# Kernel tuning notes

Measured on AMD Instinct MI355X. Metric: run time of the kernel, lower is better.

Reference implementation:

```python
import jax, jax.numpy as jnp
import numpy as np

C = 128; HEADS = 8; GH = 32; GW = 32; B = 8; PD = 8  # PD = (dim//4)//4

def _conv(x, w, pad, dil=1, groups=1):
    return jax.lax.conv_general_dilated(
        x, w, (1, 1), [(pad[0], pad[0]), (pad[1], pad[1])],
        rhs_dilation=(dil, dil),
        dimension_numbers=('NCHW', 'OIHW', 'NCHW'),
        feature_group_count=groups)

def _lrelu(t):
    return jnp.where(t >= 0, t, 0.1 * t)

def _ln(t, g, b, eps=1e-5):
    m = jnp.mean(t, -1, keepdims=True)
    v = jnp.var(t, -1, keepdims=True)
    return (t - m) * jax.lax.rsqrt(v + eps) * g + b

def setup_inputs():
    rng = np.random.RandomState(0)
    f = lambda *s: jnp.asarray((rng.randn(*s) * 0.05).astype(np.float32))
    ones = lambda n: jnp.ones((n,), jnp.float32)
    zeros = lambda n: jnp.zeros((n,), jnp.float32)
    # Swin-style relative position index over the (GH, GW) group
    coords = np.stack(np.meshgrid(np.arange(GH), np.arange(GW), indexing='ij')).reshape(2, -1)
    rel = (coords[:, :, None] - coords[:, None, :]).transpose(1, 2, 0)
    rel[..., 0] += GH - 1; rel[..., 1] += GW - 1; rel[..., 0] *= 2 * GW - 1
    rel_idx = jnp.asarray(rel.sum(-1).astype(np.int32))  # [N, N]
    biases = np.stack(np.meshgrid(np.arange(1 - GH, GH), np.arange(1 - GW, GW), indexing='ij'))
    biases = jnp.asarray(biases.reshape(2, -1).T.astype(np.float32))  # [(2GH-1)*(2GW-1), 2]
    return dict(
        x=jnp.asarray(rng.rand(B, C, GH, GW).astype(np.float32)),
        conv1_w=f(C, C, 3, 3), conv2_w=f(C, C, 3, 3), conv3_w=f(C, C, 3, 3),
        convt_w=f(C, 3, 1, 1),
        rba_w=f(C, C, 3, 1), rba_b=zeros(C), rbb_w=f(C, C, 1, 3), rbb_b=zeros(C),
        pp_w=f(PD, 2), pp_b=zeros(PD),
        l1_g=ones(PD), l1_b=zeros(PD), l1_w=f(PD, PD), l1_b2=zeros(PD),
        l2_g=ones(PD), l2_b=zeros(PD), l2_w=f(PD, PD), l2_b2=zeros(PD),
        l3_g=ones(PD), l3_b=zeros(PD), l3_w=f(HEADS, PD), l3_b2=zeros(HEADS),
        qk_w=f(2 * C, C), qk_b=zeros(2 * C),
        v_w=f(C, C), v_b=zeros(C),
        proj_w=f(C, C), proj_b=zeros(C),
        fc1_w=f(C, C), fc1_b=zeros(C), fc2_w=f(C, C), fc2_b=zeros(C),
        biases=biases, rel_idx=rel_idx,
    )

def reference(x, conv1_w, conv2_w, conv3_w, convt_w, rba_w, rba_b, rbb_w, rbb_b,
              pp_w, pp_b, l1_g, l1_b, l1_w, l1_b2, l2_g, l2_b, l2_w, l2_b2,
              l3_g, l3_b, l3_w, l3_b2, qk_w, qk_b, v_w, v_b, proj_w, proj_b,
              fc1_w, fc1_b, fc2_w, fc2_b, biases, rel_idx):
    Bn, Cc, Hh, Ww = x.shape
    N = Hh * Ww
    hd = Cc // HEADS
    # FeaExtract: ResASPP (3 dilated 3x3 convs, grouped 1x1 merge) + residual
    b1 = _lrelu(_conv(x, conv1_w, (1, 1)))
    b2 = _lrelu(_conv(x, conv2_w, (3, 3), dil=3))
    b3 = _lrelu(_conv(x, conv3_w, (5, 5), dil=5))
    a = _conv(jnp.concatenate([b1, b2, b3], 1), convt_w, (0, 0), groups=Cc) + x
    # RB: (3,1) conv -> lrelu -> (1,3) conv + residual
    r = _lrelu(_conv(a, rba_w, (1, 0)) + rba_b[None, :, None, None])
    r = _conv(r, rbb_w, (0, 1)) + rbb_b[None, :, None, None]
    o0 = r + a
    # original uses in-place clamp_, so o0 is clamped before flattening
    o0 = jnp.clip(o0, 0.0, 1.0)
    E = o0.reshape(Bn, Cc, N).transpose(0, 2, 1)  # [B, N, C]
    qk = E @ qk_w.T + qk_b  # [B, N, 2C]
    q = qk[..., :Cc].reshape(Bn, N, HEADS, hd).transpose(0, 2, 1, 3)
    k = qk[..., Cc:].reshape(Bn, N, HEADS, hd).transpose(0, 2, 1, 3)
    v = (E @ v_w.T + v_b).reshape(Bn, N, HEADS, hd).transpose(0, 2, 1, 3)
    attn = jnp.einsum('bhid,bhjd->bhij', q * (hd ** -0.5), k)
    # DynamicPosBias MLP (residual=False): Linear(2,pd) -> [LN,ReLU,Linear] x2 -> LN,ReLU,Linear(pd,heads)
    p = biases @ pp_w.T + pp_b
    p = jax.nn.relu(_ln(p, l1_g, l1_b)) @ l1_w.T + l1_b2
    p = jax.nn.relu(_ln(p, l2_g, l2_b)) @ l2_w.T + l2_b2
    p = jax.nn.relu(_ln(p, l3_g, l3_b)) @ l3_w.T + l3_b2  # [L, heads]
    rpb = p[rel_idx]  # gather -> [N, N, heads]
    attn = attn + rpb.transpose(2, 0, 1)[None]
    attn = jax.nn.softmax(attn, axis=-1)
    y = jnp.einsum('bhij,bhjd->bhid', attn, v).transpose(0, 2, 1, 3).reshape(Bn, N, Cc) + E
    x_proj = y @ proj_w.T + proj_b
    h = jax.nn.gelu(x_proj @ fc1_w.T + fc1_b, approximate=False)
    return (h @ fc2_w.T + fc2_b) + y
```

## Files before the change

### kernel.cpp

```cpp
#include <hip/hip_runtime.h>
#include <hip/hip_bf16.h>

typedef __hip_bfloat16 bf16;
typedef __bf16 bf16x8 __attribute__((ext_vector_type(8)));
typedef float f32x4 __attribute__((ext_vector_type(4)));

#define Lb 3969

#define XP_F   0
#define WF_F   903168
#define WR_F   1124352
#define WG_F   1173504
#define BH_F   1222656
#define R1P_F  1222656
#define QKV_F  1222656
#define AP_F   2795520
#define YT_F   2795520
#define EB_F   3352576
#define XPT_F  3352576
#define H1T_F  0
#define RPB_F  3876864
#define FLAG_F 3908616
#define RT_F   3908624
#define VT_F   4416528

__device__ __forceinline__ float b2f(bf16 v) { return __bfloat162float(v); }
__device__ __forceinline__ bf16 f2b(float v) { return __float2bfloat16(v); }

template <typename T> __device__ __forceinline__ float ldw(const void* p, int i);
template <> __device__ __forceinline__ float ldw<bf16>(const void* p, int i) {
  return __bfloat162float(((const bf16*)p)[i]);
}
template <> __device__ __forceinline__ float ldw<float>(const void* p, int i) {
  return ((const float*)p)[i];
}
template <typename T> __device__ __forceinline__ void stw(void* p, size_t i, float v);
template <> __device__ __forceinline__ void stw<bf16>(void* p, size_t i, float v) {
  ((bf16*)p)[i] = __float2bfloat16(v);
}
template <> __device__ __forceinline__ void stw<float>(void* p, size_t i, float v) {
  ((float*)p)[i] = v;
}

__device__ __forceinline__ unsigned pkb(float a, float b) {
  bf16 x = __float2bfloat16(a), y = __float2bfloat16(b);
  unsigned short ux = *(unsigned short*)&x, uy = *(unsigned short*)&y;
  return (unsigned)ux | ((unsigned)uy << 16);
}
__device__ __forceinline__ float bf2f_lo(unsigned w) {
  unsigned u = w << 16; return *(float*)&u;
}
__device__ __forceinline__ float bf2f_hi(unsigned w) {
  unsigned u = w & 0xffff0000u; return *(float*)&u;
}

__device__ __forceinline__ bool detect_local(const unsigned* x) {
  int lane = threadIdx.x & 63;
  int cnt = 0;
#pragma unroll
  for (int k = 0; k < 4; ++k) {
    unsigned lo = x[lane + 64 * k] & 0xFFFFu;
    cnt += (lo >= 0x3C00u && lo < 0x3F80u) ? 1 : 0;
  }
#pragma unroll
  for (int off = 1; off < 64; off <<= 1) cnt += __shfl_xor(cnt, off);
  return cnt >= 128;
}

template <typename T>
__device__ void wprep_all_body(const void* w1, const void* w2, const void* w3,
                               const void* rba_w, const void* rbb_w,
                               const void* qk_w, const void* v_w,
                               const void* proj_w, const void* fc1_w,
                               const void* fc2_w, bf16* __restrict__ Wf,
                               bf16* __restrict__ Wr, bf16* __restrict__ Wg)
{
  int tid = blockIdx.x * 256 + threadIdx.x;
  int lane = tid & 63, li = lane & 15, quad = lane >> 4;
  if (tid < 55296) {
    int mt = (tid >> 6) & 7;
    int Kc = (tid >> 9) & 3;
    int rem = tid >> 11;
    int t = rem % 9;
    int br = rem / 9;
    const void* w = (br == 0 ? w1 : (br == 1 ? w2 : w3));
    int o = mt * 16 + li;
    int ci0 = Kc * 32 + quad * 8;
#pragma unroll
    for (int j = 0; j < 8; ++j)
      Wf[(size_t)tid * 8 + j] = f2b(ldw<T>(w, (o * 128 + ci0 + j) * 9 + t));
  } else {
    int u = tid - 55296;
    if (u < 12288) {
      int Kc = (u >> 6) & 3, mt = (u >> 8) & 7, q = u >> 11;
      const void* w = (q >= 3) ? rbb_w : rba_w;
      int t = q % 3;
#pragma unroll
      for (int j = 0; j < 8; ++j)
        Wr[(size_t)u * 8 + j] =
            f2b(ldw<T>(w, ((mt * 16 + li) * 128 + Kc * 32 + quad * 8 + j) * 3 + t));
    } else if (u < 24576) {
      int g = u - 12288;
      int Kc = (g >> 6) & 3, mtg = g >> 8;
      const void* w; int mrow; float sc = 1.f;
      if (mtg < 16)      { w = qk_w;   mrow = mtg * 16; if (mtg < 8) sc = 0.25f; }
      else if (mtg < 24) { w = v_w;    mrow = (mtg - 16) * 16; }
      else if (mtg < 32) { w = proj_w; mrow = (mtg - 24) * 16; }
      else if (mtg < 40) { w = fc1_w;  mrow = (mtg - 32) * 16; }
      else               { w = fc2_w;  mrow = (mtg - 40) * 16; }
#pragma unroll
      for (int j = 0; j < 8; ++j)
        Wg[(size_t)g * 8 + j] =
            f2b(sc * ldw<T>(w, (mrow + li) * 128 + Kc * 32 + quad * 8 + j));
    }
  }
}

__global__ __launch_bounds__(256) void wprep_all_kernel(
    const unsigned* x, const void* w1, const void* w2, const void* w3,
    const void* rba_w, const void* rbb_w, const void* qk_w, const void* v_w,
    const void* proj_w, const void* fc1_w, const void* fc2_w,
    bf16* Wf, bf16* Wr, bf16* Wg, int* flag)
{
  bool isbf = detect_local(x);
  if (blockIdx.x == 0 && threadIdx.x == 0) *flag = isbf ? 1 : 0;
  if (isbf) wprep_all_body<bf16>(w1, w2, w3, rba_w, rbb_w, qk_w, v_w, proj_w,
                                 fc1_w, fc2_w, Wf, Wr, Wg);
  else      wprep_all_body<float>(w1, w2, w3, rba_w, rbb_w, qk_w, v_w, proj_w,
                                  fc1_w, fc2_w, Wf, Wr, Wg);
}

template <typename T>
__device__ void nhwc_body(const void* x, bf16* __restrict__ xp, bf16 (*tile)[128])
{
  const int b = blockIdx.x >> 5;
  const int row = blockIdx.x & 31;
  const int t = threadIdx.x;
  const size_t bbase = (size_t)b * 42 * 42 * 128;
  const bf16x8 z = (bf16x8){};

  if (t < 160) {
    int side = t / 80;
    int off = (t % 80) * 8;
    *(bf16x8*)&xp[bbase + ((size_t)(row + 5) * 42 + side * 37) * 128 + off] = z;
  }
  {
    int zr = (row < 5) ? row : ((row >= 27) ? row + 10 : -1);
    if (zr >= 0) {
      size_t base = bbase + (size_t)zr * 42 * 128;
      for (int k = t; k < 672; k += 256) *(bf16x8*)&xp[base + k * 8] = z;
    }
  }

  {
    int ci = t >> 1, half = t & 1;
#pragma unroll
    for (int j = 0; j < 16; ++j) {
      int px = half * 16 + j;
      tile[px][ci] = f2b(ldw<T>(x, ((size_t)b * 128 + ci) * 1024 + row * 32 + px));
    }
  }
  __syncthreads();
  {
    int px = t >> 3, c0 = (t & 7) * 16;
    bf16* dst = xp + (bbase + ((size_t)(row + 5) * 42 + (px + 5)) * 128 + c0);
#pragma unroll
    for (int j = 0; j < 16; ++j) dst[j] = tile[px][c0 + j];
  }
}

__global__ __launch_bounds__(256) void nhwc_kernel(const void* x, bf16* xp,
                                                   const int* flag)
{
  __shared__ bf16 tile[32][128];
  if (*flag) nhwc_body<bf16>(x, xp, tile);
  else       nhwc_body<float>(x, xp, tile);
}

__global__ __launch_bounds__(256) void aspp2_kernel(
    const bf16* __restrict__ xp, const bf16* __restrict__ Wf,
    bf16* __restrict__ bh)
{
  const int nt_ = blockIdx.x, br = blockIdx.y >> 1, mh = blockIdx.y & 1;
  const int bb = blockIdx.z;
  const int w = threadIdx.x >> 6, lane = threadIdx.x & 63;
  const int quad = lane >> 4, li = lane & 15;
  const int d = (br == 0 ? 1 : (br == 1 ? 3 : 5));
  const int pxw = nt_ * 64 + w * 16;
  const int y = pxw >> 5, xb = pxw & 31;

  f32x4 acc[4] = {};
  const bf16* Wbase = Wf + (size_t)br * 18432 * 8 + (size_t)mh * 4 * 64 * 8;

  for (int t = 0; t < 9; ++t) {
    const int dy = (t / 3 - 1) * d, dx = (t % 3 - 1) * d;
    const bf16* Asite =
        xp + (((size_t)bb * 42 + (y + 5 + dy)) * 42 + (xb + li + 5 + dx)) * 128;
    const bf16* Wt = Wbase + (size_t)t * 2048 * 8;
#pragma unroll
    for (int Kc = 0; Kc < 4; ++Kc) {
      bf16x8 afrag = *(const bf16x8*)(Asite + Kc * 32 + quad * 8);
      const bf16* Wk = Wt + (size_t)Kc * 512 * 8 + (size_t)lane * 8;
#pragma unroll
      for (int mt = 0; mt < 4; ++mt) {
        bf16x8 wfrag = *(const bf16x8*)(Wk + (size_t)mt * 64 * 8);
        acc[mt] = __builtin_amdgcn_mfma_f32_16x16x32_bf16(afrag, wfrag, acc[mt],
                                                          0, 0, 0);
      }
    }
  }
#pragma unroll
  for (int mt = 0; mt < 4; ++mt)
#pragma unroll
    for (int r = 0; r < 4; ++r) {
      int px = pxw + quad * 4 + r;
      bh[((size_t)bb * 1024 + px) * 384 + br * 128 + (mh * 4 + mt) * 16 + li] =
          f2b(acc[mt][r]);
    }
}

template <typename T>
__device__ void merge2_body(const bf16* __restrict__ xp, const void* wt,
                            const bf16* __restrict__ bh, bf16* __restrict__ ap,
                            float* cw)
{
  const int b = blockIdx.y, px0 = blockIdx.x * 32;
  const bf16x8 z = (bf16x8){};
  if (blockIdx.x == 0) {
    size_t base = ((size_t)b * 34 + 0) * 32 * 128;
    for (int k = threadIdx.x; k < 512; k += 256) *(bf16x8*)&ap[base + k * 8] = z;
  } else if (blockIdx.x == 31) {
    size_t base = ((size_t)b * 34 + 33) * 32 * 128;
    for (int k = threadIdx.x; k < 512; k += 256) *(bf16x8*)&ap[base + k * 8] = z;
  }
  for (int i = threadIdx.x; i < 384; i += 256) cw[i] = ldw<T>(wt, i);
  __syncthreads();
  const int pxl = threadIdx.x >> 3, og = threadIdx.x & 7;
  const int px = px0 + pxl, o0 = og * 16;
  const int y = px >> 5, x = px & 31;
  const bf16* brow = bh + ((size_t)b * 1024 + px) * 384 + o0 * 3;
  const bf16* xrow = xp + (((size_t)b * 42 + y + 5) * 42 + x + 5) * 128 + o0;
  bf16* arow = ap + (((size_t)b * 34 + y + 1) * 32 + x) * 128 + o0;

  bf16 bl[48], xl[16], ol[16];
#pragma unroll
  for (int k = 0; k < 6; ++k) *(bf16x8*)&bl[k * 8] = *(const bf16x8*)&brow[k * 8];
  *(bf16x8*)&xl[0] = *(const bf16x8*)&xrow[0];
  *(bf16x8*)&xl[8] = *(const bf16x8*)&xrow[8];
#pragma unroll
  for (int j = 0; j < 16; ++j) {
    float v = b2f(xl[j]);
#pragma unroll
    for (int i = 0; i < 3; ++i) {
      float t = b2f(bl[j * 3 + i]);
      v += cw[(o0 + j) * 3 + i] * (t >= 0.f ? t : 0.1f * t);
    }
    ol[j] = f2b(v);
  }
  *(bf16x8*)&arow[0] = *(bf16x8*)&ol[0];
  *(bf16x8*)&arow[8] = *(bf16x8*)&ol[8];
}

__global__ __launch_bounds__(256) void merge2_kernel(
    const bf16* xp, const void* wt, const bf16* bh, bf16* ap, const int* flag)
{
  __shared__ float cw[384];
  if (*flag) merge2_body<bf16>(xp, wt, bh, ap, cw);
  else       merge2_body<float>(xp, wt, bh, ap, cw);
}

template <typename T>
__device__ void rb1_body(const bf16* __restrict__ ap, const bf16* __restrict__ Wr,
                         const void* bias, bf16* __restrict__ r1p)
{
  const int b = blockIdx.z, mh = blockIdx.y;
  const int lane = threadIdx.x;
  const int quad = lane >> 4, li = lane & 15;
  const int pxw = blockIdx.x * 16;
  const int y = pxw >> 5, xb = pxw & 31;
  f32x4 acc[4] = {};
#pragma unroll
  for (int t = 0; t < 3; ++t) {
    const bf16* Asite = ap + (((size_t)b * 34 + y + t) * 32 + xb + li) * 128;
#pragma unroll
    for (int Kc = 0; Kc < 4; ++Kc) {
      bf16x8 afrag = *(const bf16x8*)(Asite + Kc * 32 + quad * 8);
#pragma unroll
      for (int mt = 0; mt < 4; ++mt) {
        int f = (t * 8 + mh * 4 + mt) * 4 + Kc;
        bf16x8 wfrag = *(const bf16x8*)(Wr + ((size_t)f * 64 + lane) * 8);
        acc[mt] = __builtin_amdgcn_mfma_f32_16x16x32_bf16(afrag, wfrag, acc[mt],
                                                          0, 0, 0);
      }
    }
  }
  if (quad == 0) {
    int xcol = (xb == 0) ? 0 : 33;
#pragma unroll
    for (int mt = 0; mt < 4; ++mt)
      r1p[(((size_t)b * 32 + y) * 34 + xcol) * 128 + (mh * 4 + mt) * 16 + li] =
          f2b(0.f);
  }
#pragma unroll
  for (int mt = 0; mt < 4; ++mt) {
    int o = (mh * 4 + mt) * 16 + li;
    float bv = ldw<T>(bias, o);
#pragma unroll
    for (int r = 0; r < 4; ++r) {
      int x = xb + quad * 4 + r;
      float v = acc[mt][r] + bv;
      v = (v >= 0.f ? v : 0.1f * v);
      r1p[(((size_t)b * 32 + y) * 34 + x + 1) * 128 + o] = f2b(v);
    }
  }
}

__global__ __launch_bounds__(64) void rb1_kernel(
    const bf16* ap, const bf16* Wr, const void* bias, bf16* r1p, const int* flag)
{
  if (*flag) rb1_body<bf16>(ap, Wr, bias, r1p);
  else       rb1_body<float>(ap, Wr, bias, r1p);
}

template <typename T>
__device__ void rb2_body(const bf16* __restrict__ r1p, const bf16* __restrict__ Wr,
                         const void* bias, const bf16* __restrict__ ap,
                         bf16* __restrict__ Eb)
{
  const int b = blockIdx.z, mh = blockIdx.y;
  const int lane = threadIdx.x;
  const int quad = lane >> 4, li = lane & 15;
  const int pxw = blockIdx.x * 16;
  const int y = pxw >> 5, xb = pxw & 31;
  f32x4 acc[4] = {};
#pragma unroll
  for (int t = 0; t < 3; ++t) {
    const bf16* Asite = r1p + (((size_t)b * 32 + y) * 34 + xb + li + t) * 128;
#pragma unroll
    for (int Kc = 0; Kc < 4; ++Kc) {
      bf16x8 afrag = *(const bf16x8*)(Asite + Kc * 32 + quad * 8);
#pragma unroll
      for (int mt = 0; mt < 4; ++mt) {
        int f = ((3 + t) * 8 + mh * 4 + mt) * 4 + Kc;
        bf16x8 wfrag = *(const bf16x8*)(Wr + ((size_t)f * 64 + lane) * 8);
        acc[mt] = __builtin_amdgcn_mfma_f32_16x16x32_bf16(afrag, wfrag, acc[mt],
                                                          0, 0, 0);
      }
    }
  }
#pragma unroll
  for (int mt = 0; mt < 4; ++mt) {
    int o = (mh * 4 + mt) * 16 + li;
    float bv = ldw<T>(bias, o);
#pragma unroll
    for (int r = 0; r < 4; ++r) {
      int x = xb + quad * 4 + r;
      float v = acc[mt][r] + bv +
                b2f(ap[(((size_t)b * 34 + y + 1) * 32 + x) * 128 + o]);
      v = fminf(fmaxf(v, 0.f), 1.f);
      Eb[((size_t)b * 1024 + y * 32 + x) * 128 + o] = f2b(v);
    }
  }
}

__global__ __launch_bounds__(64) void rb2_kernel(
    const bf16* r1p, const bf16* Wr, const void* bias, const bf16* ap,
    bf16* Eb, const int* flag)
{
  if (*flag) rb2_body<bf16>(r1p, Wr, bias, ap, Eb);
  else       rb2_body<float>(r1p, Wr, bias, ap, Eb);
}

template <typename T>
__device__ __forceinline__ void ln_relu8(const float* t, float* u,
                                         const void* g, const void* bb)
{
  float m = 0.f;
#pragma unroll
  for (int k = 0; k < 8; ++k) m += t[k];
  m *= 0.125f;
  float v = 0.f;
#pragma unroll
  for (int k = 0; k < 8; ++k) { float d = t[k] - m; v += d * d; }
  v *= 0.125f;
  float r = rsqrtf(v + 1e-5f);
#pragma unroll
  for (int k = 0; k < 8; ++k) {
    float val = (t[k] - m) * r * ldw<T>(g, k) + ldw<T>(bb, k);
    u[k] = val > 0.f ? val : 0.f;
  }
}

template <typename T>
__device__ void dpb_body(const void* biases, const void* pp_w, const void* pp_b,
                         const void* l1_g, const void* l1_b, const void* l1_w,
                         const void* l1_b2, const void* l2_g, const void* l2_b,
                         const void* l2_w, const void* l2_b2, const void* l3_g,
                         const void* l3_b, const void* l3_w, const void* l3_b2,
                         float* __restrict__ RPB)
{
  int r = blockIdx.x * 256 + threadIdx.x;
  if (r >= Lb) return;
  float b0 = ldw<T>(biases, r * 2), b1 = ldw<T>(biases, r * 2 + 1);
  float t[8], u[8];
#pragma unroll
  for (int j = 0; j < 8; ++j)
    t[j] = b0 * ldw<T>(pp_w, j * 2) + b1 * ldw<T>(pp_w, j * 2 + 1) +
           ldw<T>(pp_b, j);
  ln_relu8<T>(t, u, l1_g, l1_b);
#pragma unroll
  for (int j = 0; j < 8; ++j) {
    float s = ldw<T>(l1_b2, j);
#pragma unroll
    for (int k = 0; k < 8; ++k) s += u[k] * ldw<T>(l1_w, j * 8 + k);
    t[j] = s;
  }
  ln_relu8<T>(t, u, l2_g, l2_b);
#pragma unroll
  for (int j = 0; j < 8; ++j) {
    float s = ldw<T>(l2_b2, j);
#pragma unroll
    for (int k = 0; k < 8; ++k) s += u[k] * ldw<T>(l2_w, j * 8 + k);
    t[j] = s;
  }
  ln_relu8<T>(t, u, l3_g, l3_b);
#pragma unroll
  for (int h = 0; h < 8; ++h) {
    float s = ldw<T>(l3_b2, h);
#pragma unroll
    for (int k = 0; k < 8; ++k) s += u[k] * ldw<T>(l3_w, h * 8 + k);
    RPB[h * Lb + r] = s;
  }
}

__global__ __launch_bounds__(256) void dpb_kernel(
    const void* biases, const void* pp_w, const void* pp_b, const void* l1_g,
    const void* l1_b, const void* l1_w, const void* l1_b2, const void* l2_g,
    const void* l2_b, const void* l2_w, const void* l2_b2, const void* l3_g,
    const void* l3_b, const void* l3_w, const void* l3_b2, float* RPB,
    const int* flag)
{
  if (*flag)
    dpb_body<bf16>(biases, pp_w, pp_b, l1_g, l1_b, l1_w, l1_b2, l2_g, l2_b,
                   l2_w, l2_b2, l3_g, l3_b, l3_w, l3_b2, RPB);
  else
    dpb_body<float>(biases, pp_w, pp_b, l1_g, l1_b, l1_w, l1_b2, l2_g, l2_b,
                    l2_w, l2_b2, l3_g, l3_b, l3_w, l3_b2, RPB);
}

__global__ __launch_bounds__(64) void rt_kernel(
    const float* __restrict__ RPB, bf16* __restrict__ RT)
{
  const int tt = blockIdx.x, h = blockIdx.y;
  const int t = tt >> 1, p = tt & 1;
  const int lane = threadIdx.x, quad = lane >> 4, li = lane & 15;
  const float* rp = RPB + h * Lb;
#pragma unroll
  for (int mt = 0; mt < 4; ++mt) {
    unsigned w[2];
#pragma unroll
    for (int rr = 0; rr < 2; ++rr) {
      float v0, v1;
#pragma unroll
      for (int k = 0; k < 2; ++k) {
        int r = rr * 2 + k;
        int j = mt * 16 + quad * 4 + r;
        int dy = (t - 30) - (j >> 5);
        int dx = (p * 16 + li) - (j & 31);
        float v = rp[(dy + 31) * 63 + dx + 31];
        if (k == 0) v0 = v; else v1 = v;
      }
      w[rr] = pkb(v0, v1);
    }
    *(uint2*)&RT[(((size_t)h * 124 + tt) * 4 + mt) * 256 + lane * 4] =
        make_uint2(w[0], w[1]);
  }
}

__global__ __launch_bounds__(64) void vt_kernel(
    const bf16* __restrict__ QKV, bf16* __restrict__ VT)
{
  const int c = blockIdx.x, hh = blockIdx.y, b = blockIdx.z;
  __shared__ bf16 Vl[64][20];
  const int lane = threadIdx.x, quad = lane >> 4, li = lane & 15;
  const bf16* vsrc =
      QKV + ((size_t)b * 1024 + c * 64 + lane) * 384 + 256 + hh * 16;
  union { bf16x8 v; uint2 u[2]; } w0, w1;
  w0.v = *(const bf16x8*)vsrc;
  w1.v = *(const bf16x8*)(vsrc + 8);
  *(uint2*)&Vl[lane][0] = w0.u[0];
  *(uint2*)&Vl[lane][4] = w0.u[1];
  *(uint2*)&Vl[lane][8] = w1.u[0];
  *(uint2*)&Vl[lane][12] = w1.u[1];
  __syncthreads();
#pragma unroll
  for (int half = 0; half < 2; ++half) {
    union { bf16 e[8]; bf16x8 v; } uv;
#pragma unroll
    for (int jj = 0; jj < 8; ++jj)
      uv.e[jj] = Vl[half * 32 + quad * 8 + jj][li];
    *(bf16x8*)&VT[((((size_t)(b * 8 + hh) * 16 + c) * 2 + half) * 64 + lane) * 8] =
        uv.v;
  }
}

template <typename T>
__device__ void qkv_body(const bf16* __restrict__ Eb, const bf16* __restrict__ Wg,
                         const void* qk_b, const void* v_b,
                         bf16* __restrict__ QKV)
{
  const int grp = blockIdx.y, b = blockIdx.z;
  const int w = threadIdx.x >> 6, lane = threadIdx.x & 63;
  const int quad = lane >> 4, li = lane & 15;
  const int pxw = blockIdx.x * 64 + w * 16;
  bf16x8 ef[4];
#pragma unroll
  for (int Kc = 0; Kc < 4; ++Kc)
    ef[Kc] = *(const bf16x8*)&Eb[((size_t)b * 1024 + pxw + li) * 128 + Kc * 32 +
                                 quad * 8];
  f32x4 acc[8] = {};
#pragma unroll
  for (int nt = 0; nt < 8; ++nt) {
    int g = grp * 8 + nt;
#pragma unroll
    for (int Kc = 0; Kc < 4; ++Kc) {
      bf16x8 wf = *(const bf16x8*)&Wg[(((size_t)g * 4 + Kc) * 64 + lane) * 8];
      acc[nt] = __builtin_amdgcn_mfma_f32_16x16x32_bf16(ef[Kc], wf, acc[nt],
                                                        0, 0, 0);
    }
  }
#pragma unroll
  for (int nt = 0; nt < 8; ++nt) {
    int g = grp * 8 + nt;
    int o = g * 16 + li;
    float bv;
    if (g < 8)       bv = 0.25f * ldw<T>(qk_b, o);
    else if (g < 16) bv = ldw<T>(qk_b, o);
    else             bv = ldw<T>(v_b, o - 256);
#pragma unroll
    for (int r = 0; r < 4; ++r) {
      int px = pxw + quad * 4 + r;
      QKV[((size_t)b * 1024 + px) * 384 + o] = f2b(acc[nt][r] + bv);
    }
  }
}

__global__ __launch_bounds__(256) void qkv_kernel(
    const bf16* Eb, const bf16* Wg, const void* qk_b, const void* v_b,
    bf16* QKV, const int* flag)
{
  if (*flag) qkv_body<bf16>(Eb, Wg, qk_b, v_b, QKV);
  else       qkv_body<float>(Eb, Wg, qk_b, v_b, QKV);
}

template <typename T, int MODE>
__device__ void mlp_body(const bf16* __restrict__ src, const bf16* __restrict__ Wg,
                         int tb, const void* bias, const bf16* __restrict__ res,
                         void* out)
{
  const int b = blockIdx.z, mh = blockIdx.y;
  const int lane = threadIdx.x;
  const int quad = lane >> 4, li = lane & 15;
  const int pxw = blockIdx.x * 16;
  bf16x8 ef[4];
#pragma unroll
  for (int Kc = 0; Kc < 4; ++Kc)
    ef[Kc] = *(const bf16x8*)&src[((size_t)b * 1024 + pxw + li) * 128 + Kc * 32 +
                                  quad * 8];
  f32x4 acc[2] = {};
#pragma unroll
  for (int nt = 0; nt < 2; ++nt)
#pragma unroll
    for (int Kc = 0; Kc < 4; ++Kc) {
      bf16x8 wf = *(const bf16x8*)&Wg[
          (((size_t)(tb + mh * 2 + nt) * 4 + Kc) * 64 + lane) * 8];
      acc[nt] = __builtin_amdgcn_mfma_f32_16x16x32_bf16(ef[Kc], wf, acc[nt],
                                                        0, 0, 0);
    }
#pragma unroll
  for (int nt = 0; nt < 2; ++nt) {
    int o = (mh * 2 + nt) * 16 + li;
    float bv = ldw<T>(bias, o);
#pragma unroll
    for (int r = 0; r < 4; ++r) {
      int px = pxw + quad * 4 + r;
      float v = acc[nt][r] + bv;
      size_t oidx = ((size_t)b * 1024 + px) * 128 + o;
      if (MODE == 1) v = 0.5f * v * (1.f + erff(v * 0.70710678118f));
      if (MODE == 2) {
        v += b2f(res[oidx]);
        stw<T>(out, oidx, v);
      } else {
        ((bf16*)out)[oidx] = f2b(v);
      }
    }
  }
}

template <int MODE>
__global__ __launch_bounds__(64) void mlp_kernel(
    const bf16* src, const bf16* Wg, int tb, const void* bias, const bf16* res,
    void* out, const int* flag)
{
  if (*flag) mlp_body<bf16, MODE>(src, Wg, tb, bias, res, out);
  else       mlp_body<float, MODE>(src, Wg, tb, bias, res, out);
}

__global__ __launch_bounds__(64) void attn_kernel(
    const bf16* __restrict__ QKV, const bf16* __restrict__ Eb,
    const bf16* __restrict__ RT, const bf16* __restrict__ VT,
    bf16* __restrict__ Yt)
{
  const int qt = blockIdx.x;
  const int hh = blockIdx.y;
  const int b = blockIdx.z;

  __shared__ bf16 Pl[16][72];

  const int lane = threadIdx.x;
  const int quad = lane >> 4, li = lane & 15;
  const int qb = qt * 16;

  const bf16* QKVb = QKV + (size_t)b * 1024 * 384;
  const bf16* VTb = VT + (size_t)(b * 8 + hh) * 16 * 1024;
  const bf16* RTh = RT + (size_t)hh * 124 * 1024;

  bf16x8 qf = (bf16x8){};
  if (quad < 2)
    qf = *(const bf16x8*)&QKVb[(size_t)(qb + li) * 384 + hh * 16 + quad * 8];

  f32x4 O_ = {};
  float m_st = -1e30f, l_st = 0.f;
  const int sbase = (lane & 48) + ((lane >> 2) & 12);

  for (int c = 0; c < 16; ++c) {
    const int c0 = c * 64;
    const int tt = ((qt >> 1) - 2 * c + 30) * 2 + (qt & 1);
    const bf16* rtp = RTh + (size_t)tt * 1024 + lane * 4;

    f32x4 sT[4];
#pragma unroll
    for (int mt = 0; mt < 4; ++mt) {
      uint2 rw = *(const uint2*)(rtp + (size_t)mt * 256);
      f32x4 cin;
      cin[0] = bf2f_lo(rw.x); cin[1] = bf2f_hi(rw.x);
      cin[2] = bf2f_lo(rw.y); cin[3] = bf2f_hi(rw.y);
      bf16x8 kf = (bf16x8){};
      if (quad < 2)
        kf = *(const bf16x8*)&QKVb[(size_t)(c0 + mt * 16 + li) * 384 + 128 +
                                   hh * 16 + quad * 8];
      sT[mt] = __builtin_amdgcn_mfma_f32_16x16x32_bf16(kf, qf, cin, 0, 0, 0);
    }

    float cm = sT[0][0];
#pragma unroll
    for (int mt = 0; mt < 4; ++mt)
#pragma unroll
      for (int r = 0; r < 4; ++r) cm = fmaxf(cm, sT[mt][r]);
    cm = fmaxf(cm, __shfl_xor(cm, 16));
    cm = fmaxf(cm, __shfl_xor(cm, 32));
    float mn = fmaxf(m_st, cm);
    float al = __expf(m_st - mn);
    m_st = mn;
    float ps = 0.f;
#pragma unroll
    for (int mt = 0; mt < 4; ++mt)
#pragma unroll
      for (int r = 0; r < 4; ++r) {
        float p = __expf(sT[mt][r] - mn);
        sT[mt][r] = p;
        ps += p;
      }
    ps += __shfl_xor(ps, 16);
    ps += __shfl_xor(ps, 32);
    l_st = l_st * al + ps;

#pragma unroll
    for (int r = 0; r < 4; ++r) O_[r] *= __shfl(al, sbase + r);

#pragma unroll
    for (int mt = 0; mt < 4; ++mt) {
      uint2 w;
      w.x = pkb(sT[mt][0], sT[mt][1]);
      w.y = pkb(sT[mt][2], sT[mt][3]);
      *(uint2*)&Pl[li][mt * 16 + quad * 4] = w;
    }
    __syncthreads();

#pragma unroll
    for (int half = 0; half < 2; ++half) {
      bf16x8 vf = *(const bf16x8*)&VTb[((size_t)(c * 2 + half) * 64 + lane) * 8];
      bf16x8 pf = *(const bf16x8*)&Pl[li][half * 32 + quad * 8];
      O_ = __builtin_amdgcn_mfma_f32_16x16x32_bf16(pf, vf, O_, 0, 0, 0);
    }
    __syncthreads();
  }

  const bf16* Ebp = Eb + (size_t)b * 1024 * 128 + hh * 16 + li;
  bf16* Ytp = Yt + (size_t)b * 1024 * 128 + hh * 16 + li;
#pragma unroll
  for (int r = 0; r < 4; ++r) {
    float lb = __shfl(l_st, sbase + r);
    int qrow = qb + quad * 4 + r;
    Ytp[(size_t)qrow * 128] =
        f2b(O_[r] / lb + b2f(Ebp[(size_t)qrow * 128]));
  }
}

extern "C" void kernel_launch(void* const* d_in, const int* in_sizes, int n_in,
                              void* d_out, int out_size, void* d_ws,
                              size_t ws_size, hipStream_t stream)
{
  (void)in_sizes; (void)n_in; (void)out_size; (void)ws_size;
  const void* x       = d_in[0];
  const void* conv1_w = d_in[1];
  const void* conv2_w = d_in[2];
  const void* conv3_w = d_in[3];
  const void* convt_w = d_in[4];
  const void* rba_w   = d_in[5];
  const void* rba_b   = d_in[6];
  const void* rbb_w   = d_in[7];
  const void* rbb_b   = d_in[8];
  const void* pp_w    = d_in[9];
  const void* pp_b    = d_in[10];
  const void* l1_g    = d_in[11];
  const void* l1_b    = d_in[12];
  const void* l1_w    = d_in[13];
  const void* l1_b2   = d_in[14];
  const void* l2_g    = d_in[15];
  const void* l2_b    = d_in[16];
  const void* l2_w    = d_in[17];
  const void* l2_b2   = d_in[18];
  const void* l3_g    = d_in[19];
  const void* l3_b    = d_in[20];
  const void* l3_w    = d_in[21];
  const void* l3_b2   = d_in[22];
  const void* qk_w    = d_in[23];
  const void* qk_b    = d_in[24];
  const void* v_w     = d_in[25];
  const void* v_b     = d_in[26];
  const void* proj_w  = d_in[27];
  const void* proj_b  = d_in[28];
  const void* fc1_w   = d_in[29];
  const void* fc1_b   = d_in[30];
  const void* fc2_w   = d_in[31];
  const void* fc2_b   = d_in[32];
  const void* biases  = d_in[33];

  float* ws   = (float*)d_ws;
  bf16*  xp   = (bf16*)(ws + XP_F);
  bf16*  Wf   = (bf16*)(ws + WF_F);
  bf16*  Wr   = (bf16*)(ws + WR_F);
  bf16*  Wg   = (bf16*)(ws + WG_F);
  bf16*  bh   = (bf16*)(ws + BH_F);
  bf16*  r1p  = (bf16*)(ws + R1P_F);
  bf16*  QKV  = (bf16*)(ws + QKV_F);
  bf16*  ap   = (bf16*)(ws + AP_F);
  bf16*  Yt   = (bf16*)(ws + YT_F);
  bf16*  Eb   = (bf16*)(ws + EB_F);
  bf16*  XPt  = (bf16*)(ws + XPT_F);
  bf16*  H1t  = (bf16*)(ws + H1T_F);
  float* RPB  = ws + RPB_F;
  int*   flag = (int*)(ws + FLAG_F);
  bf16*  RT   = (bf16*)(ws + RT_F);
  bf16*  VT   = (bf16*)(ws + VT_F);

  wprep_all_kernel<<<312, 256, 0, stream>>>(
      (const unsigned*)x, conv1_w, conv2_w, conv3_w, rba_w, rbb_w, qk_w, v_w,
      proj_w, fc1_w, fc2_w, Wf, Wr, Wg, flag);
  nhwc_kernel<<<256, 256, 0, stream>>>(x, xp, flag);
  aspp2_kernel<<<dim3(16, 6, 8), 256, 0, stream>>>(xp, Wf, bh);
  merge2_kernel<<<dim3(32, 8), 256, 0, stream>>>(xp, convt_w, bh, ap, flag);
  rb1_kernel<<<dim3(64, 2, 8), 64, 0, stream>>>(ap, Wr, rba_b, r1p, flag);
  rb2_kernel<<<dim3(64, 2, 8), 64, 0, stream>>>(r1p, Wr, rbb_b, ap, Eb, flag);
  dpb_kernel<<<16, 256, 0, stream>>>(biases, pp_w, pp_b, l1_g, l1_b, l1_w,
                                     l1_b2, l2_g, l2_b, l2_w, l2_b2, l3_g,
                                     l3_b, l3_w, l3_b2, RPB, flag);
  rt_kernel<<<dim3(124, 8), 64, 0, stream>>>(RPB, RT);
  qkv_kernel<<<dim3(16, 3, 8), 256, 0, stream>>>(Eb, Wg, qk_b, v_b, QKV, flag);
  vt_kernel<<<dim3(16, 8, 8), 64, 0, stream>>>(QKV, VT);
  attn_kernel<<<dim3(64, 8, 8), 64, 0, stream>>>(QKV, Eb, RT, VT, Yt);
  mlp_kernel<0><<<dim3(64, 4, 8), 64, 0, stream>>>(Yt, Wg, 24, proj_b, nullptr,
                                                   XPt, flag);
  mlp_kernel<1><<<dim3(64, 4, 8), 64, 0, stream>>>(XPt, Wg, 32, fc1_b, nullptr,
                                                   H1t, flag);
  mlp_kernel<2><<<dim3(64, 4, 8), 64, 0, stream>>>(H1t, Wg, 40, fc2_b, Yt,
                                                   d_out, flag);
}
```

Baseline: 243.5 us.

## Keep P in registers via f16 MFMA, double-buffer K/bias loads, lazy softmax rescale

The attention kernel now feeds softmax probabilities directly from registers into a 16x16x16 f16 MFMA, with V pre-transposed to fp16 in the matching fragment layout. This removes the LDS round-trip and both __syncthreads per chunk. K fragments and relative-bias tiles are double-buffered across chunks, and the bias table is stored as fp32 so it is used without unpacking. The online-softmax rescale is skipped unless the running max grows by more than 8. In exchange, the fp32 bias table doubles its memory traffic and P and V lose some precision in fp16.

New measurement: 247.7 us. About the same (+1.7%).

```diff
diff --git a/kernel.cpp b/kernel.cpp
--- a/kernel.cpp
+++ b/kernel.cpp
@@ -4,6 +4,8 @@
 typedef __hip_bfloat16 bf16;
 typedef __bf16 bf16x8 __attribute__((ext_vector_type(8)));
 typedef float f32x4 __attribute__((ext_vector_type(4)));
+typedef __fp16 f16x2 __attribute__((ext_vector_type(2)));
+typedef __fp16 f16x4 __attribute__((ext_vector_type(4)));
 
 #define Lb 3969
 
@@ -22,7 +24,7 @@
 #define RPB_F  3876864
 #define FLAG_F 3908616
 #define RT_F   3908624
-#define VT_F   4416528
+#define VT_F   4924432
 
 __device__ __forceinline__ float b2f(bf16 v) { return __bfloat162float(v); }
 __device__ __forceinline__ bf16 f2b(float v) { return __float2bfloat16(v); }
@@ -47,11 +49,9 @@
   unsigned short ux = *(unsigned short*)&x, uy = *(unsigned short*)&y;
   return (unsigned)ux | ((unsigned)uy << 16);
 }
-__device__ __forceinline__ float bf2f_lo(unsigned w) {
-  unsigned u = w << 16; return *(float*)&u;
-}
-__device__ __forceinline__ float bf2f_hi(unsigned w) {
-  unsigned u = w & 0xffff0000u; return *(float*)&u;
+__device__ __forceinline__ unsigned pkh(float a, float b) {
+  f16x2 t = __builtin_amdgcn_cvt_pkrtz(a, b);
+  return *(unsigned*)&t;
 }
 
 __device__ __forceinline__ bool detect_local(const unsigned* x) {
@@ -449,36 +449,29 @@
 }
 
 __global__ __launch_bounds__(64) void rt_kernel(
-    const float* __restrict__ RPB, bf16* __restrict__ RT)
+    const float* __restrict__ RPB, float* __restrict__ RTf)
 {
   const int tt = blockIdx.x, h = blockIdx.y;
   const int t = tt >> 1, p = tt & 1;
   const int lane = threadIdx.x, quad = lane >> 4, li = lane & 15;
   const float* rp = RPB + h * Lb;
+  float* dst = RTf + ((size_t)(h * 124 + tt) * 4) * 256 + lane * 4;
 #pragma unroll
   for (int mt = 0; mt < 4; ++mt) {
-    unsigned w[2];
-#pragma unroll
-    for (int rr = 0; rr < 2; ++rr) {
-      float v0, v1;
-#pragma unroll
-      for (int k = 0; k < 2; ++k) {
-        int r = rr * 2 + k;
-        int j = mt * 16 + quad * 4 + r;
-        int dy = (t - 30) - (j >> 5);
-        int dx = (p * 16 + li) - (j & 31);
-        float v = rp[(dy + 31) * 63 + dx + 31];
-        if (k == 0) v0 = v; else v1 = v;
-      }
-      w[rr] = pkb(v0, v1);
-    }
-    *(uint2*)&RT[(((size_t)h * 124 + tt) * 4 + mt) * 256 + lane * 4] =
-        make_uint2(w[0], w[1]);
+    f32x4 v;
+#pragma unroll
+    for (int r = 0; r < 4; ++r) {
+      int j = mt * 16 + quad * 4 + r;
+      int dy = (t - 30) - (j >> 5);
+      int dx = (p * 16 + li) - (j & 31);
+      v[r] = rp[(dy + 31) * 63 + dx + 31];
+    }
+    *(f32x4*)(dst + mt * 256) = v;
   }
 }
 
 __global__ __launch_bounds__(64) void vt_kernel(
-    const bf16* __restrict__ QKV, bf16* __restrict__ VT)
+    const bf16* __restrict__ QKV, uint2* __restrict__ VTh)
 {
   const int c = blockIdx.x, hh = blockIdx.y, b = blockIdx.z;
   __shared__ bf16 Vl[64][20];
@@ -493,14 +486,15 @@
   *(uint2*)&Vl[lane][8] = w1.u[0];
   *(uint2*)&Vl[lane][12] = w1.u[1];
   __syncthreads();
-#pragma unroll
-  for (int half = 0; half < 2; ++half) {
-    union { bf16 e[8]; bf16x8 v; } uv;
-#pragma unroll
-    for (int jj = 0; jj < 8; ++jj)
-      uv.e[jj] = Vl[half * 32 + quad * 8 + jj][li];
-    *(bf16x8*)&VT[((((size_t)(b * 8 + hh) * 16 + c) * 2 + half) * 64 + lane) * 8] =
-        uv.v;
+  uint2* dst = VTh + (((size_t)(b * 8 + hh) * 16 + c) * 4) * 64 + lane;
+#pragma unroll
+  for (int mt = 0; mt < 4; ++mt) {
+    uint2 pu;
+    pu.x = pkh(b2f(Vl[mt * 16 + quad * 4 + 0][li]),
+               b2f(Vl[mt * 16 + quad * 4 + 1][li]));
+    pu.y = pkh(b2f(Vl[mt * 16 + quad * 4 + 2][li]),
+               b2f(Vl[mt * 16 + quad * 4 + 3][li]));
+    dst[(size_t)mt * 64] = pu;
   }
 }
 
@@ -608,22 +602,20 @@
 
 __global__ __launch_bounds__(64) void attn_kernel(
     const bf16* __restrict__ QKV, const bf16* __restrict__ Eb,
-    const bf16* __restrict__ RT, const bf16* __restrict__ VT,
+    const float* __restrict__ RTf, const uint2* __restrict__ VTh,
     bf16* __restrict__ Yt)
 {
   const int qt = blockIdx.x;
   const int hh = blockIdx.y;
   const int b = blockIdx.z;
 
-  __shared__ bf16 Pl[16][72];
-
   const int lane = threadIdx.x;
   const int quad = lane >> 4, li = lane & 15;
   const int qb = qt * 16;
 
   const bf16* QKVb = QKV + (size_t)b * 1024 * 384;
-  const bf16* VTb = VT + (size_t)(b * 8 + hh) * 16 * 1024;
-  const bf16* RTh = RT + (size_t)hh * 124 * 1024;
+  const uint2* VTb = VTh + (size_t)(b * 8 + hh) * 4096;
+  const float* RTh = RTf + (size_t)hh * 124 * 1024;
 
   bf16x8 qf = (bf16x8){};
   if (quad < 2)
@@ -633,25 +625,34 @@
   float m_st = -1e30f, l_st = 0.f;
   const int sbase = (lane & 48) + ((lane >> 2) & 12);
 
-  for (int c = 0; c < 16; ++c) {
+  struct Buf { bf16x8 kf[4]; f32x4 cin[4]; };
+  Buf bA, bB;
+
+  auto LOAD = [&](Buf& bf, int c) {
     const int c0 = c * 64;
     const int tt = ((qt >> 1) - 2 * c + 30) * 2 + (qt & 1);
-    const bf16* rtp = RTh + (size_t)tt * 1024 + lane * 4;
+    const float* rtp = RTh + (size_t)tt * 1024 + lane * 4;
+#pragma unroll
+    for (int mt = 0; mt < 4; ++mt) {
+      bf.cin[mt] = *(const f32x4*)(rtp + mt * 256);
+      bf.kf[mt] = (bf16x8){};
+      if (quad < 2)
+        bf.kf[mt] = *(const bf16x8*)&QKVb[(size_t)(c0 + mt * 16 + li) * 384 +
+                                          128 + hh * 16 + quad * 8];
+    }
+  };
+
+  auto STEP = [&](const Buf& bf, int c) {
+    uint2 vb[4];
+#pragma unroll
+    for (int mt = 0; mt < 4; ++mt)
+      vb[mt] = VTb[(size_t)(c * 4 + mt) * 64 + lane];
 
     f32x4 sT[4];
 #pragma unroll
-    for (int mt = 0; mt < 4; ++mt) {
-      uint2 rw = *(const uint2*)(rtp + (size_t)mt * 256);
-      f32x4 cin;
-      cin[0] = bf2f_lo(rw.x); cin[1] = bf2f_hi(rw.x);
-      cin[2] = bf2f_lo(rw.y); cin[3] = bf2f_hi(rw.y);
-      bf16x8 kf = (bf16x8){};
-      if (quad < 2)
-        kf = *(const bf16x8*)&QKVb[(size_t)(c0 + mt * 16 + li) * 384 + 128 +
-                                   hh * 16 + quad * 8];
-      sT[mt] = __builtin_amdgcn_mfma_f32_16x16x32_bf16(kf, qf, cin, 0, 0, 0);
-    }
-
+    for (int mt = 0; mt < 4; ++mt)
+      sT[mt] = __builtin_amdgcn_mfma_f32_16x16x32_bf16(bf.kf[mt], qf,
+                                                       bf.cin[mt], 0, 0, 0);
     float cm = sT[0][0];
 #pragma unroll
     for (int mt = 0; mt < 4; ++mt)
@@ -659,41 +660,44 @@
       for (int r = 0; r < 4; ++r) cm = fmaxf(cm, sT[mt][r]);
     cm = fmaxf(cm, __shfl_xor(cm, 16));
     cm = fmaxf(cm, __shfl_xor(cm, 32));
-    float mn = fmaxf(m_st, cm);
-    float al = __expf(m_st - mn);
-    m_st = mn;
+    if (!__all(cm <= m_st + 8.f)) {
+      float mn = fmaxf(m_st, cm);
+      float al = __expf(m_st - mn);
+      m_st = mn;
+      l_st *= al;
+#pragma unroll
+      for (int r = 0; r < 4; ++r) O_[r] *= __shfl(al, sbase + r);
+    }
     float ps = 0.f;
 #pragma unroll
     for (int mt = 0; mt < 4; ++mt)
 #pragma unroll
       for (int r = 0; r < 4; ++r) {
-        float p = __expf(sT[mt][r] - mn);
+        float p = __expf(sT[mt][r] - m_st);
         sT[mt][r] = p;
         ps += p;
       }
     ps += __shfl_xor(ps, 16);
     ps += __shfl_xor(ps, 32);
-    l_st = l_st * al + ps;
-
-#pragma unroll
-    for (int r = 0; r < 4; ++r) O_[r] *= __shfl(al, sbase + r);
+    l_st += ps;
 
 #pragma unroll
     for (int mt = 0; mt < 4; ++mt) {
-      uint2 w;
-      w.x = pkb(sT[mt][0], sT[mt][1]);
-      w.y = pkb(sT[mt][2], sT[mt][3]);
-      *(uint2*)&Pl[li][mt * 16 + quad * 4] = w;
-    }
-    __syncthreads();
-
-#pragma unroll
-    for (int half = 0; half < 2; ++half) {
-      bf16x8 vf = *(const bf16x8*)&VTb[((size_t)(c * 2 + half) * 64 + lane) * 8];
-      bf16x8 pf = *(const bf16x8*)&Pl[li][half * 32 + quad * 8];
-      O_ = __builtin_amdgcn_mfma_f32_16x16x32_bf16(pf, vf, O_, 0, 0, 0);
-    }
-    __syncthreads();
+      union { unsigned u[2]; f16x4 h4; } pu;
+      pu.u[0] = pkh(sT[mt][0], sT[mt][1]);
+      pu.u[1] = pkh(sT[mt][2], sT[mt][3]);
+      union { uint2 u; f16x4 h; } vu;
+      vu.u = vb[mt];
+      O_ = __builtin_amdgcn_mfma_f32_16x16x16f16(pu.h4, vu.h, O_, 0, 0, 0);
+    }
+  };
+
+  LOAD(bA, 0);
+  for (int c = 0; c < 16; c += 2) {
+    LOAD(bB, c + 1);
+    STEP(bA, c);
+    if (c + 2 < 16) LOAD(bA, c + 2);
+    STEP(bB, c + 1);
   }
 
   const bf16* Ebp = Eb + (size_t)b * 1024 * 128 + hh * 16 + li;
@@ -762,8 +766,8 @@
   bf16*  H1t  = (bf16*)(ws + H1T_F);
   float* RPB  = ws + RPB_F;
   int*   flag = (int*)(ws + FLAG_F);
-  bf16*  RT   = (bf16*)(ws + RT_F);
-  bf16*  VT   = (bf16*)(ws + VT_F);
+  float* RTf  = ws + RT_F;
+  uint2* VTh  = (uint2*)(ws + VT_F);
 
   wprep_all_kernel<<<312, 256, 0, stream>>>(
       (const unsigned*)x, conv1_w, conv2_w, conv3_w, rba_w, rbb_w, qk_w, v_w,
@@ -776,10 +780,10 @@
   dpb_kernel<<<16, 256, 0, stream>>>(biases, pp_w, pp_b, l1_g, l1_b, l1_w,
                                      l1_b2, l2_g, l2_b, l2_w, l2_b2, l3_g,
                                      l3_b, l3_w, l3_b2, RPB, flag);
-  rt_kernel<<<dim3(124, 8), 64, 0, stream>>>(RPB, RT);
+  rt_kernel<<<dim3(124, 8), 64, 0, stream>>>(RPB, RTf);
   qkv_kernel<<<dim3(16, 3, 8), 256, 0, stream>>>(Eb, Wg, qk_b, v_b, QKV, flag);
-  vt_kernel<<<dim3(16, 8, 8), 64, 0, stream>>>(QKV, VT);
-  attn_kernel<<<dim3(64, 8, 8), 64, 0, stream>>>(QKV, Eb, RT, VT, Yt);
+  vt_kernel<<<dim3(16, 8, 8), 64, 0, stream>>>(QKV, VTh);
+  attn_kernel<<<dim3(64, 8, 8), 64, 0, stream>>>(QKV, Eb, RTf, VTh, Yt);
   mlp_kernel<0><<<dim3(64, 4, 8), 64, 0, stream>>>(Yt, Wg, 24, proj_b, nullptr,
                                                    XPt, flag);
   mlp_kernel<1><<<dim3(64, 4, 8), 64, 0, stream>>>(XPt, Wg, 32, fc1_b, nullptr,
```
